# Kernel tuning notes

Measured on AMD Instinct MI355X. Metric: run time of the kernel, lower is better.

The kernel has to match this reference:

```python
import jax, jax.numpy as jnp
import numpy as np

N_NODES = 100000
N_EDGES = 1600000
N_GRAPHS = 512


def gcn_conv(x, row, col, W, b):
    # x: [N, Cin], row/col: [E] (self-loops already appended)
    n = x.shape[0]
    h = x @ W                                        # [N, Cout]
    deg = jax.ops.segment_sum(jnp.ones_like(col, dtype=x.dtype), col, num_segments=n)
    dinv = jnp.where(deg > 0, deg ** -0.5, 0.0)
    norm = dinv[row] * dinv[col]                     # [E]
    msg = norm[:, None] * h[row]                     # [E, Cout]
    out = jax.ops.segment_sum(msg, col, num_segments=n)
    return out + b


def setup_inputs() -> dict:
    key = jax.random.key(0)
    ks = jax.random.split(key, 10)
    x = jax.random.normal(ks[0], (N_NODES, 128), dtype=jnp.float32)
    edge_index = jax.random.randint(ks[1], (2, N_EDGES), 0, N_NODES, dtype=jnp.int64)
    batch = jnp.sort(jax.random.randint(ks[2], (N_NODES,), 0, N_GRAPHS, dtype=jnp.int64))
    def lin_w(k, fan_in, fan_out):
        bound = 1.0 / np.sqrt(fan_in)
        return jax.random.uniform(k, (fan_in, fan_out), jnp.float32, -bound, bound)
    # GCN layers (bias zero-initialized per reset_parameters)
    W1 = lin_w(ks[3], 128, 128); b1 = jnp.zeros((128,), jnp.float32)
    W2 = lin_w(ks[4], 128, 128); b2 = jnp.zeros((128,), jnp.float32)
    # MLP layers (Linear with bias)
    Wm1 = lin_w(ks[5], 128, 64)
    bm1 = jax.random.uniform(ks[6], (64,), jnp.float32, -1/np.sqrt(128), 1/np.sqrt(128))
    Wm2 = lin_w(ks[7], 64, 1)
    bm2 = jax.random.uniform(ks[8], (1,), jnp.float32, -1/np.sqrt(64), 1/np.sqrt(64))
    return {"x": x, "edge_index": edge_index, "batch": batch,
            "W1": W1, "b1": b1, "W2": W2, "b2": b2,
            "Wm1": Wm1, "bm1": bm1, "Wm2": Wm2, "bm2": bm2}


def reference(x, edge_index, batch, W1, b1, W2, b2, Wm1, bm1, Wm2, bm2):
    n = x.shape[0]
    loops = jnp.arange(n, dtype=edge_index.dtype)
    row = jnp.concatenate([edge_index[0], loops])
    col = jnp.concatenate([edge_index[1], loops])
    # GCN: conv -> relu -> conv
    h = gcn_conv(x, row, col, W1, b1)
    h = jax.nn.relu(h)
    h = gcn_conv(h, row, col, W2, b2)
    # scatter-mean pooling over graphs
    sums = jax.ops.segment_sum(h, batch, num_segments=N_GRAPHS)      # [G, C]
    counts = jax.ops.segment_sum(jnp.ones((n,), h.dtype), batch, num_segments=N_GRAPHS)
    g = sums / jnp.maximum(counts, 1.0)[:, None]
    # MLP: linear -> relu -> linear
    g = jax.nn.relu(g @ Wm1 + bm1)
    out = g @ Wm2 + bm2
    return out
```

## Files before the change

### kernel.cpp

```cpp
#include <hip/hip_runtime.h>
#include <math.h>

#define C_DIM 128
#define POOL_CHUNK 64
#define BKT_SHIFT 7
#define MAX_B 1024
#define CB 256
#define CHUNK_MAX 6400
#define FB_CAP 8192
typedef unsigned short ushort_t;
typedef __attribute__((ext_vector_type(8))) short short8;
typedef __attribute__((ext_vector_type(4))) float f32x4;
typedef __attribute__((ext_vector_type(2))) float f32x2;

static inline int ceil_div(int a, int b) { return (a + b - 1) / b; }

__device__ inline ushort_t f2bf(float f) {
    union { float f; unsigned u; } v; v.f = f;
    unsigned r = v.u + 0x7FFFu + ((v.u >> 16) & 1u);
    return (ushort_t)(r >> 16);
}
__device__ inline float bf_lo(unsigned u) {
    union { unsigned v; float f; } c; c.v = u << 16; return c.f;
}
__device__ inline float bf_hi(unsigned u) {
    union { unsigned v; float f; } c; c.v = u & 0xFFFF0000u; return c.f;
}
__device__ inline void accum8pk(uint4 u, f32x2 ac[4]) {
    ac[0] += (f32x2){bf_lo(u.x), bf_hi(u.x)};
    ac[1] += (f32x2){bf_lo(u.y), bf_hi(u.y)};
    ac[2] += (f32x2){bf_lo(u.z), bf_hi(u.z)};
    ac[3] += (f32x2){bf_lo(u.w), bf_hi(u.w)};
}

__global__ __launch_bounds__(512) void k_sortchunk(
    const int* __restrict__ row, const int* __restrict__ col, int E, int chunk,
    int B, int* __restrict__ counts, int* __restrict__ sstart,
    int* __restrict__ epk,
    const float* __restrict__ W1, const float* __restrict__ W2,
    uint4* __restrict__ wf1, uint4* __restrict__ wf2,
    float* __restrict__ gsums, int GC, int* __restrict__ cursor) {
    int t = threadIdx.x, blk = blockIdx.x;
    if (blk >= CB) {
        const float* W = (blk == CB) ? W1 : W2;
        uint4* wf = (blk == CB) ? wf1 : wf2;
        for (int f = t; f < 2048; f += 512) {
            int lane = f & 63, kkn = f >> 6;
            int kk = kkn & 3, nt = kkn >> 2;
            int n = lane & 15, quad = lane >> 4;
            union { ushort_t h[8]; uint4 v; } u;
#pragma unroll
            for (int j = 0; j < 8; ++j)
                u.h[j] = f2bf(W[(size_t)(kk * 32 + quad * 8 + j) * C_DIM + nt * 16 + n]);
            wf[f] = u.v;
        }
        return;
    }
    for (int i = blk * 512 + t; i < GC; i += CB * 512) gsums[i] = 0.f;
    if (blk == 0 && t == 0) *cursor = 0;

    __shared__ int hist[MAX_B];
    __shared__ int hscan[MAX_B];
    __shared__ int sd[512];
    __shared__ __align__(16) int ebuf[CHUNK_MAX];
    __shared__ __align__(8)  ushort_t bbuf[CHUNK_MAX];
    __shared__ int sorted[CHUNK_MAX];

    for (int i = t; i < B; i += 512) hist[i] = 0;
    __syncthreads();
    int s = blk * chunk;
    int e = s + chunk; if (e > E) e = E;
    int cnt = e - s;
    for (int i = s + 4 * t; i < e; i += 2048) {
        int4 c = *(const int4*)(col + i);
        int4 r = *(const int4*)(row + i);
        int li = i - s;
        int4 pk;
        pk.x = (r.x << 7) | (c.x & 127);
        pk.y = (r.y << 7) | (c.y & 127);
        pk.z = (r.z << 7) | (c.z & 127);
        pk.w = (r.w << 7) | (c.w & 127);
        *(int4*)&ebuf[li] = pk;
        ushort4 bk;
        bk.x = (ushort_t)(c.x >> BKT_SHIFT);
        bk.y = (ushort_t)(c.y >> BKT_SHIFT);
        bk.z = (ushort_t)(c.z >> BKT_SHIFT);
        bk.w = (ushort_t)(c.w >> BKT_SHIFT);
        *(ushort4*)&bbuf[li] = bk;
        atomicAdd(&hist[bk.x], 1);
        atomicAdd(&hist[bk.y], 1);
        atomicAdd(&hist[bk.z], 1);
        atomicAdd(&hist[bk.w], 1);
    }
    __syncthreads();
    {
        int base2 = t * 2;
        int vv[2]; int sum = 0;
#pragma unroll
        for (int j = 0; j < 2; ++j) {
            int idx = base2 + j;
            vv[j] = (idx < B) ? hist[idx] : 0;
            sum += vv[j];
        }
        sd[t] = sum;
        __syncthreads();
        for (int off = 1; off < 512; off <<= 1) {
            int x = (t >= off) ? sd[t - off] : 0;
            __syncthreads();
            sd[t] += x;
            __syncthreads();
        }
        int run = sd[t] - sum;
#pragma unroll
        for (int j = 0; j < 2; ++j) {
            int idx = base2 + j;
            if (idx < B) hscan[idx] = run;
            run += vv[j];
        }
    }
    __syncthreads();
    for (int i = t; i < B; i += 512) {
        counts[(size_t)blk * MAX_B + i] = hist[i];
        sstart[(size_t)blk * MAX_B + i] = hscan[i];
    }
    __syncthreads();
    for (int i = t; i < B; i += 512) hist[i] = hscan[i];
    __syncthreads();
    for (int i = t; i < cnt; i += 512) {
        int pos = atomicAdd(&hist[bbuf[i]], 1);
        sorted[pos] = ebuf[i];
    }
    __syncthreads();
    for (int i = t; i * 4 < cnt; i += 512)
        *(int4*)&epk[s + i * 4] = *(const int4*)&sorted[i * 4];
}

__global__ __launch_bounds__(256) void k_bfinal(
    const int* __restrict__ epk, const int* __restrict__ counts,
    const int* __restrict__ sstart, int* __restrict__ cursor,
    int chunk, int N,
    int2* __restrict__ offs2, float* __restrict__ dinv, int* __restrict__ csr) {
    __shared__ int sh[FB_CAP];
    __shared__ int sd[256];
    __shared__ int cnt[128];
    __shared__ int pre[128];
    __shared__ int cur[128];
    __shared__ int sbase_s;
    int bkt = blockIdx.x, t = threadIdx.x;
    int base = bkt << BKT_SHIFT;
    int nn = N - base; if (nn > 128) nn = 128;

    int segln = counts[(size_t)t * MAX_B + bkt];
    int gs = t * chunk + sstart[(size_t)t * MAX_B + bkt];
    sd[t] = segln;
    __syncthreads();
    for (int off = 1; off < 256; off <<= 1) {
        int x = (t >= off) ? sd[t - off] : 0;
        __syncthreads();
        sd[t] += x;
        __syncthreads();
    }
    int place = sd[t] - segln;
    int m = sd[255];
    if (t < 128) cnt[t] = 0;
    __syncthreads();

    bool fits = (m <= FB_CAP);
    if (fits) {
        for (int j = 0; j < segln; ++j) {
            int u = epk[gs + j];
            sh[place + j] = u;
            atomicAdd(&cnt[u & 127], 1);
        }
    } else {
        for (int j = 0; j < segln; ++j)
            atomicAdd(&cnt[epk[gs + j] & 127], 1);
    }
    __syncthreads();
    if (t < 128) pre[t] = (cnt[t] + 3) & ~3;
    __syncthreads();
    for (int off = 1; off < 128; off <<= 1) {
        int x = (t >= off && t < 128) ? pre[t - off] : 0;
        __syncthreads();
        if (t < 128) pre[t] += x;
        __syncthreads();
    }
    if (t == 127) sbase_s = atomicAdd(cursor, pre[127]);
    __syncthreads();
    int sbase = sbase_s;
    if (t < 128) {
        int c4 = (cnt[t] + 3) & ~3;
        int ex = pre[t] - c4;
        cur[t] = ex;
        if (t < nn) {
            offs2[base + t] = make_int2(sbase + ex, sbase + ex + c4);
            dinv[base + t] = 1.0f / sqrtf((float)cnt[t] + 1.0f);
        }
    }
    __syncthreads();
    if (fits) {
        for (int i = t; i < m; i += 256) {
            int u = sh[i];
            int slot = atomicAdd(&cur[u & 127], 1);
            csr[sbase + slot] = (u >> 7) << 8;
        }
    } else {
        for (int j = 0; j < segln; ++j) {
            int u = epk[gs + j];
            int slot = atomicAdd(&cur[u & 127], 1);
            csr[sbase + slot] = (u >> 7) << 8;
        }
    }
    __syncthreads();
    if (t < nn) {
        int c4 = (cnt[t] + 3) & ~3;
        int ex = pre[t] - c4;
        int zoff = N << 8;
        for (int k2 = cnt[t]; k2 < c4; ++k2) csr[sbase + ex + k2] = zoff;
    }
}

template <int ABF16>
__global__ __launch_bounds__(256) void k_matmul_mfma(
    const float* __restrict__ Af, const ushort_t* __restrict__ Abf,
    const uint4* __restrict__ wfrag, const float* __restrict__ dinv,
    ushort_t* __restrict__ Cb, int N) {
    __shared__ uint4 wfs[2048];
    __shared__ __align__(16) ushort_t As[64 * 136];
    int t = threadIdx.x;
    int wv = t >> 6, lane = t & 63;
    int n = lane & 15, quad = lane >> 4;
    int row0 = blockIdx.x * 64;

    for (int i = t; i < 2048; i += 256) wfs[i] = wfrag[i];

    if (ABF16) {
#pragma unroll
        for (int i = 0; i < 4; ++i) {
            int idx = i * 256 + t;
            int r = idx >> 4, c8 = idx & 15;
            int grow = row0 + r; if (grow >= N) grow = N - 1;
            uint4 u = *(const uint4*)(Abf + (size_t)grow * C_DIM + c8 * 8);
            *(uint4*)&As[r * 136 + c8 * 8] = u;
        }
    } else {
#pragma unroll
        for (int i = 0; i < 8; ++i) {
            int idx = i * 256 + t;
            int r = idx >> 5, cq = idx & 31;
            int grow = row0 + r; if (grow >= N) grow = N - 1;
            float4 f = *(const float4*)(Af + (size_t)grow * C_DIM + cq * 4);
            union { ushort_t h[4]; uint2 v; } c;
            c.h[0] = f2bf(f.x); c.h[1] = f2bf(f.y);
            c.h[2] = f2bf(f.z); c.h[3] = f2bf(f.w);
            *(uint2*)&As[r * 136 + cq * 4] = c.v;
        }
    }

    f32x4 acc[8];
#pragma unroll
    for (int i = 0; i < 8; ++i) acc[i] = (f32x4){0.f, 0.f, 0.f, 0.f};

    __syncthreads();

    int rl = wv * 16 + n;
#pragma unroll
    for (int kk = 0; kk < 4; ++kk) {
        union { uint4 v; short8 s; } ca;
        ca.v = *(const uint4*)&As[rl * 136 + kk * 32 + quad * 8];
#pragma unroll
        for (int nt = 0; nt < 8; ++nt) {
            union { uint4 v; short8 s; } cb;
            cb.v = wfs[(nt * 4 + kk) * 64 + lane];
            acc[nt] = __builtin_amdgcn_mfma_f32_16x16x32_bf16(ca.s, cb.s, acc[nt], 0, 0, 0);
        }
    }

    __syncthreads();
#pragma unroll
    for (int reg = 0; reg < 4; ++reg) {
        int lr = wv * 16 + quad * 4 + reg;
        int grow = row0 + lr;
        float sc = dinv[grow < N ? grow : N - 1];
#pragma unroll
        for (int nt = 0; nt < 8; ++nt)
            As[lr * 136 + nt * 16 + n] = f2bf(acc[nt][reg] * sc);
    }
    __syncthreads();
    int rows = N - row0; if (rows > 64) rows = 64;
    for (int idx = t; idx < 16 * 64; idx += 256) {
        int r = idx >> 4, c8 = idx & 15;
        if (r < rows)
            *(uint4*)(Cb + (size_t)(row0 + r) * C_DIM + c8 * 8) =
                *(const uint4*)&As[r * 136 + c8 * 8];
        else if (row0 + r == N)
            *(uint4*)(Cb + (size_t)N * C_DIM + c8 * 8) = (uint4){0, 0, 0, 0};
    }
}

template <int RELU>
__global__ __launch_bounds__(256) void k_aggregate(
    const ushort_t* __restrict__ hs, const int2* __restrict__ offs2,
    const int* __restrict__ csr, const float* __restrict__ dinv,
    const float* __restrict__ bias, uint4* __restrict__ outV, int N) {
    int t = threadIdx.x & 63;
    int half = t >> 5;
    int q2 = (t >> 4) & 1;
    int fs = t & 15;
    int node = (blockIdx.x << 3) + ((threadIdx.x >> 6) << 1) + half;
    bool valid = node < N;
    if (!valid) node = N - 1;
    const char* hb = (const char*)hs;
    unsigned fso = (unsigned)(fs << 4);
    int2 se = offs2[node];
    int j = se.x, e = se.y;

    f32x2 ac[4];
    if (q2 == 0) {
        uint4 u = *(const uint4*)(hb + ((unsigned)node << 8) + fso);
        ac[0] = (f32x2){bf_lo(u.x), bf_hi(u.x)};
        ac[1] = (f32x2){bf_lo(u.y), bf_hi(u.y)};
        ac[2] = (f32x2){bf_lo(u.z), bf_hi(u.z)};
        ac[3] = (f32x2){bf_lo(u.w), bf_hi(u.w)};
    } else {
#pragma unroll
        for (int i = 0; i < 4; ++i) ac[i] = (f32x2){0.f, 0.f};
    }

    for (; j + 16 <= e; j += 16) {
        const int4* cp = (const int4*)(csr + j + (q2 << 3));
        int4 ra = cp[0];
        int4 rb = cp[1];
        uint4 u0 = *(const uint4*)(hb + (unsigned)ra.x + fso);
        uint4 u1 = *(const uint4*)(hb + (unsigned)ra.y + fso);
        uint4 u2 = *(const uint4*)(hb + (unsigned)ra.z + fso);
        uint4 u3 = *(const uint4*)(hb + (unsigned)ra.w + fso);
        uint4 u4 = *(const uint4*)(hb + (unsigned)rb.x + fso);
        uint4 u5 = *(const uint4*)(hb + (unsigned)rb.y + fso);
        uint4 u6 = *(const uint4*)(hb + (unsigned)rb.z + fso);
        uint4 u7 = *(const uint4*)(hb + (unsigned)rb.w + fso);
        accum8pk(u0, ac); accum8pk(u1, ac);
        accum8pk(u2, ac); accum8pk(u3, ac);
        accum8pk(u4, ac); accum8pk(u5, ac);
        accum8pk(u6, ac); accum8pk(u7, ac);
    }
    if (j + 8 <= e) {
        int4 ra = *(const int4*)(csr + j + (q2 << 2));
        uint4 u0 = *(const uint4*)(hb + (unsigned)ra.x + fso);
        uint4 u1 = *(const uint4*)(hb + (unsigned)ra.y + fso);
        uint4 u2 = *(const uint4*)(hb + (unsigned)ra.z + fso);
        uint4 u3 = *(const uint4*)(hb + (unsigned)ra.w + fso);
        accum8pk(u0, ac); accum8pk(u1, ac);
        accum8pk(u2, ac); accum8pk(u3, ac);
        j += 8;
    }
    if (j + 4 <= e) {
        int2 rc = *(const int2*)(csr + j + (q2 << 1));
        uint4 u0 = *(const uint4*)(hb + (unsigned)rc.x + fso);
        uint4 u1 = *(const uint4*)(hb + (unsigned)rc.y + fso);
        accum8pk(u0, ac); accum8pk(u1, ac);
    }

#pragma unroll
    for (int i = 0; i < 4; ++i) {
        ac[i].x += __shfl_xor(ac[i].x, 16);
        ac[i].y += __shfl_xor(ac[i].y, 16);
    }

    if (q2 == 0 && valid) {
        float dn = dinv[node];
        float4 b0 = *(const float4*)(bias + fs * 8);
        float4 b1 = *(const float4*)(bias + fs * 8 + 4);
        float o[8];
        o[0] = dn * ac[0].x + b0.x; o[1] = dn * ac[0].y + b0.y;
        o[2] = dn * ac[1].x + b0.z; o[3] = dn * ac[1].y + b0.w;
        o[4] = dn * ac[2].x + b1.x; o[5] = dn * ac[2].y + b1.y;
        o[6] = dn * ac[3].x + b1.z; o[7] = dn * ac[3].y + b1.w;
        if (RELU) {
#pragma unroll
            for (int i = 0; i < 8; ++i) o[i] = fmaxf(o[i], 0.f);
        }
        uint4 pk;
        pk.x = (unsigned)f2bf(o[0]) | ((unsigned)f2bf(o[1]) << 16);
        pk.y = (unsigned)f2bf(o[2]) | ((unsigned)f2bf(o[3]) << 16);
        pk.z = (unsigned)f2bf(o[4]) | ((unsigned)f2bf(o[5]) << 16);
        pk.w = (unsigned)f2bf(o[6]) | ((unsigned)f2bf(o[7]) << 16);
        outV[(size_t)node * 16 + fs] = pk;
    }
}

__global__ __launch_bounds__(128) void k_pool_sum(
    const ushort_t* __restrict__ h, const int* __restrict__ batch, int n,
    float* __restrict__ sums) {
    int r0 = blockIdx.x * POOL_CHUNK;
    int r1 = r0 + POOL_CHUNK; if (r1 > n) r1 = n;
    if (r0 >= n) return;
    int t = threadIdx.x;
    int c = t & 63, rr = t >> 6;
    float2 acc = make_float2(0.f, 0.f);
    int g = batch[r0];
    int i = r0;
    while (i < r1) {
        if (i + 8 <= r1 && batch[i + 7] == g) {
#pragma unroll
            for (int b = 0; b < 4; ++b) {
                unsigned u = *(const unsigned*)(h + (size_t)(i + rr + 2 * b) * C_DIM + c * 2);
                acc.x += bf_lo(u); acc.y += bf_hi(u);
            }
            i += 8;
        } else {
            int bi = batch[i];
            if (bi != g) {
                atomicAdd(&sums[(size_t)g * C_DIM + c * 2], acc.x);
                atomicAdd(&sums[(size_t)g * C_DIM + c * 2 + 1], acc.y);
                acc = make_float2(0.f, 0.f); g = bi;
            }
            if (rr == 0) {
                unsigned u = *(const unsigned*)(h + (size_t)i * C_DIM + c * 2);
                acc.x += bf_lo(u); acc.y += bf_hi(u);
            }
            ++i;
        }
    }
    atomicAdd(&sums[(size_t)g * C_DIM + c * 2], acc.x);
    atomicAdd(&sums[(size_t)g * C_DIM + c * 2 + 1], acc.y);
}

__global__ __launch_bounds__(128) void k_mlp(
    const float* __restrict__ sums, const int* __restrict__ batch, int n,
    const float* __restrict__ Wm1, const float* __restrict__ bm1,
    const float* __restrict__ Wm2, const float* __restrict__ bm2,
    float* __restrict__ out) {
    int g = blockIdx.x;
    int t = threadIdx.x;
    int lo = 0, hi = n;
    while (lo < hi) { int m = (lo + hi) >> 1; if (batch[m] < g) lo = m + 1; else hi = m; }
    int start = lo;
    lo = start; hi = n;
    while (lo < hi) { int m = (lo + hi) >> 1; if (batch[m] < g + 1) lo = m + 1; else hi = m; }
    float cnt = (float)(lo - start);

    float mean = sums[(size_t)g * C_DIM + t] / fmaxf(cnt, 1.0f);

    __shared__ float m_s[128];
    __shared__ float hid[64];
    m_s[t] = mean;
    __syncthreads();
    if (t < 64) {
        float a = bm1[t];
#pragma unroll 4
        for (int k = 0; k < 128; ++k) a += m_s[k] * Wm1[k * 64 + t];
        hid[t] = fmaxf(a, 0.f) * Wm2[t];
    }
    __syncthreads();
    if (t < 64) {
        float v = hid[t];
        for (int off = 32; off > 0; off >>= 1) v += __shfl_down(v, off);
        if (t == 0) out[g] = v + bm2[0];
    }
}

extern "C" void kernel_launch(void* const* d_in, const int* in_sizes, int n_in,
                              void* d_out, int out_size, void* d_ws, size_t ws_size,
                              hipStream_t stream) {
    const float* x     = (const float*)d_in[0];
    const int*   eidx  = (const int*)d_in[1];
    const int*   batch = (const int*)d_in[2];
    const float* W1    = (const float*)d_in[3];
    const float* b1    = (const float*)d_in[4];
    const float* W2    = (const float*)d_in[5];
    const float* b2    = (const float*)d_in[6];
    const float* Wm1   = (const float*)d_in[7];
    const float* bm1   = (const float*)d_in[8];
    const float* Wm2   = (const float*)d_in[9];
    const float* bm2   = (const float*)d_in[10];

    const int N = in_sizes[2];
    const int E = in_sizes[1] / 2;
    const int G = out_size;
    const int B = (N + 127) >> BKT_SHIFT;

    char* p = (char*)d_ws;
    auto carve = [&](size_t bytes) {
        char* q = p;
        p += (bytes + 255) & ~(size_t)255;
        return q;
    };
    ushort_t* bufT   = (ushort_t*)carve((size_t)(N + 1) * C_DIM * sizeof(ushort_t));
    ushort_t* bufA   = (ushort_t*)carve((size_t)N * C_DIM * sizeof(ushort_t));
    float*    dinv   = (float*)   carve((size_t)N * sizeof(float));
    int2*     offs2  = (int2*)    carve((size_t)N * sizeof(int2));
    int*      csr    = (int*)     carve(((size_t)E + 3 * (size_t)N + 64) * sizeof(int));
    int*      counts = (int*)     carve((size_t)CB * MAX_B * sizeof(int));
    int*      sstart = (int*)     carve((size_t)CB * MAX_B * sizeof(int));
    float*    gsums  = (float*)   carve((size_t)G * C_DIM * sizeof(float));
    uint4*    wf1    = (uint4*)   carve(2048 * sizeof(uint4));
    uint4*    wf2    = (uint4*)   carve(2048 * sizeof(uint4));
    int*      cursor = (int*)     carve(sizeof(int));
    int*      epk    = (int*)bufT;

    const int* erow = eidx;
    const int* ecol = eidx + E;
    const int chunk = (ceil_div(E, CB) + 3) & ~3;

    k_sortchunk<<<CB + 2, 512, 0, stream>>>(erow, ecol, E, chunk, B,
                                            counts, sstart, epk,
                                            W1, W2, wf1, wf2, gsums, G * C_DIM, cursor);
    k_bfinal<<<B, 256, 0, stream>>>(epk, counts, sstart, cursor, chunk, N,
                                    offs2, dinv, csr);

    k_matmul_mfma<0><<<ceil_div(N, 64), 256, 0, stream>>>(x, nullptr, wf1, dinv, bufT, N);
    k_aggregate<1><<<ceil_div(N, 8), 256, 0, stream>>>(bufT, offs2, csr, dinv, b1,
                                                       (uint4*)bufA, N);
    k_matmul_mfma<1><<<ceil_div(N, 64), 256, 0, stream>>>(nullptr, bufA, wf2, dinv, bufT, N);
    k_aggregate<0><<<ceil_div(N, 8), 256, 0, stream>>>(bufT, offs2, csr, dinv, b2,
                                                       (uint4*)bufA, N);
    k_pool_sum<<<ceil_div(N, POOL_CHUNK), 128, 0, stream>>>(bufA, batch, N, gsums);
    k_mlp<<<G, 128, 0, stream>>>(gsums, batch, N, Wm1, bm1, Wm2, bm2, (float*)d_out);
}
```

Measured before the change: 306.6 us.

## Sort nodes by degree within buckets to balance aggregate warp workloads

Adds a per-bucket counting sort of the 128 nodes by in-degree (capped at 63) in the CSR finalize kernel and writes a permutation array. The aggregate kernels now map each half-wavefront to a node through this permutation, so nodes with similar degree share a wavefront and the loop trip counts diverge less. In return the finalize kernel does extra scans and atomics, there is one more indirect load per node, and neighbouring nodes in memory no longer run together. Padding slots in the last bucket repeat the last node and write its output twice with identical values.

Result: slower. 328.1 us (+7.0%).

```diff
diff --git a/kernel.cpp b/kernel.cpp
--- a/kernel.cpp
+++ b/kernel.cpp
@@ -139,12 +139,16 @@
     const int* __restrict__ epk, const int* __restrict__ counts,
     const int* __restrict__ sstart, int* __restrict__ cursor,
     int chunk, int N,
-    int2* __restrict__ offs2, float* __restrict__ dinv, int* __restrict__ csr) {
+    int2* __restrict__ offs2, float* __restrict__ dinv, int* __restrict__ csr,
+    int* __restrict__ perm) {
     __shared__ int sh[FB_CAP];
     __shared__ int sd[256];
     __shared__ int cnt[128];
     __shared__ int pre[128];
     __shared__ int cur[128];
+    __shared__ int dbin[64];
+    __shared__ int dsc[64];
+    __shared__ int dcur[64];
     __shared__ int sbase_s;
     int bkt = blockIdx.x, t = threadIdx.x;
     int base = bkt << BKT_SHIFT;
@@ -217,6 +221,29 @@
         int ex = pre[t] - c4;
         int zoff = N << 8;
         for (int k2 = cnt[t]; k2 < c4; ++k2) csr[sbase + ex + k2] = zoff;
+    }
+    __syncthreads();
+    if (t < 64) { dbin[t] = 0; dcur[t] = 0; }
+    __syncthreads();
+    int deg = 0, bidx = 0, tn = 0;
+    if (t < 128) {
+        tn = (t < nn) ? t : (nn - 1);
+        deg = cnt[tn];
+        bidx = deg > 63 ? 63 : deg;
+        atomicAdd(&dbin[bidx], 1);
+    }
+    __syncthreads();
+    if (t < 64) dsc[t] = dbin[t];
+    __syncthreads();
+    for (int off = 1; off < 64; off <<= 1) {
+        int x = (t >= off && t < 64) ? dsc[t - off] : 0;
+        __syncthreads();
+        if (t < 64) dsc[t] += x;
+        __syncthreads();
+    }
+    if (t < 128) {
+        int rank = dsc[bidx] - dbin[bidx] + atomicAdd(&dcur[bidx], 1);
+        perm[(bkt << 7) + rank] = base + tn;
     }
 }
 
@@ -302,14 +329,15 @@
 __global__ __launch_bounds__(256) void k_aggregate(
     const ushort_t* __restrict__ hs, const int2* __restrict__ offs2,
     const int* __restrict__ csr, const float* __restrict__ dinv,
-    const float* __restrict__ bias, uint4* __restrict__ outV, int N) {
+    const int* __restrict__ perm, const float* __restrict__ bias,
+    uint4* __restrict__ outV, int N) {
     int t = threadIdx.x & 63;
     int half = t >> 5;
     int q2 = (t >> 4) & 1;
     int fs = t & 15;
-    int node = (blockIdx.x << 3) + ((threadIdx.x >> 6) << 1) + half;
-    bool valid = node < N;
-    if (!valid) node = N - 1;
+    int bkt = blockIdx.x >> 4;
+    int pos = ((blockIdx.x & 15) << 3) + ((threadIdx.x >> 6) << 1) + half;
+    int node = perm[(bkt << 7) + pos];
     const char* hb = (const char*)hs;
     unsigned fso = (unsigned)(fs << 4);
     int2 se = offs2[node];
@@ -367,7 +395,7 @@
         ac[i].y += __shfl_xor(ac[i].y, 16);
     }
 
-    if (q2 == 0 && valid) {
+    if (q2 == 0) {
         float dn = dinv[node];
         float4 b0 = *(const float4*)(bias + fs * 8);
         float4 b1 = *(const float4*)(bias + fs * 8 + 4);
@@ -497,6 +525,7 @@
     uint4*    wf1    = (uint4*)   carve(2048 * sizeof(uint4));
     uint4*    wf2    = (uint4*)   carve(2048 * sizeof(uint4));
     int*      cursor = (int*)     carve(sizeof(int));
+    int*      perm   = (int*)     carve((size_t)B * 128 * sizeof(int));
     int*      epk    = (int*)bufT;
 
     const int* erow = eidx;
@@ -507,14 +536,14 @@
                                             counts, sstart, epk,
                                             W1, W2, wf1, wf2, gsums, G * C_DIM, cursor);
     k_bfinal<<<B, 256, 0, stream>>>(epk, counts, sstart, cursor, chunk, N,
-                                    offs2, dinv, csr);
+                                    offs2, dinv, csr, perm);
 
     k_matmul_mfma<0><<<ceil_div(N, 64), 256, 0, stream>>>(x, nullptr, wf1, dinv, bufT, N);
-    k_aggregate<1><<<ceil_div(N, 8), 256, 0, stream>>>(bufT, offs2, csr, dinv, b1,
-                                                       (uint4*)bufA, N);
+    k_aggregate<1><<<B * 16, 256, 0, stream>>>(bufT, offs2, csr, dinv, perm, b1,
+                                               (uint4*)bufA, N);
     k_matmul_mfma<1><<<ceil_div(N, 64), 256, 0, stream>>>(nullptr, bufA, wf2, dinv, bufT, N);
-    k_aggregate<0><<<ceil_div(N, 8), 256, 0, stream>>>(bufT, offs2, csr, dinv, b2,
-                                                       (uint4*)bufA, N);
+    k_aggregate<0><<<B * 16, 256, 0, stream>>>(bufT, offs2, csr, dinv, perm, b2,
+                                               (uint4*)bufA, N);
     k_pool_sum<<<ceil_div(N, POOL_CHUNK), 128, 0, stream>>>(bufA, batch, N, gsums);
     k_mlp<<<G, 128, 0, stream>>>(gsums, batch, N, Wm1, bm1, Wm2, bm2, (float*)d_out);
 }
```
